# Performance work log

Hardware: AMD Instinct MI355X
Metric: run time of the kernel (lower is better)

Reference implementation:

```python
import jax, jax.numpy as jnp
import numpy as np

B, N_ATOMS, N_PROBES, N_EDGES = 4, 1250, 50000, 125000
T, D, SH_DIM, NUM_BASIS = 3, 128, 16, 10
CUTOFF = 4.0
NUM_NEIGHBORS = 20.0


def spherical_harmonics_l3(u):
    """Real spherical harmonics l=0..3, component normalization (||Y_l||^2 = 2l+1 on unit vectors). u: [E,3] unit vectors."""
    x, y, z = u[:, 0], u[:, 1], u[:, 2]
    x2, y2, z2 = x * x, y * y, z * z
    s3 = np.sqrt(3.0)
    s15 = np.sqrt(15.0)
    sh = [
        jnp.ones_like(x),                       # l=0
        s3 * x, s3 * y, s3 * z,                 # l=1
        s15 * x * y,                            # l=2
        s15 * y * z,
        (np.sqrt(5.0) / 2.0) * (3.0 * z2 - 1.0),
        s15 * x * z,
        (s15 / 2.0) * (x2 - y2),
        np.sqrt(35.0 / 8.0) * y * (3.0 * x2 - y2),   # l=3
        np.sqrt(105.0) * x * y * z,
        np.sqrt(21.0 / 8.0) * y * (5.0 * z2 - 1.0),
        (np.sqrt(7.0) / 2.0) * (5.0 * z2 * z - 3.0 * z),
        np.sqrt(21.0 / 8.0) * x * (5.0 * z2 - 1.0),
        (np.sqrt(105.0) / 2.0) * z * (x2 - y2),
        np.sqrt(35.0 / 8.0) * x * (x2 - 3.0 * y2),
    ]
    return jnp.stack(sh, axis=-1)  # [E, 16]


def radial_basis(r):
    """Normalized gaussian radial basis on [0, CUTOFF] (e3nn soft_one_hot_linspace style). r: [E]."""
    centers = jnp.linspace(0.0, CUTOFF, NUM_BASIS)
    step = CUTOFF / (NUM_BASIS - 1)
    diff = (r[:, None] - centers) / step
    return jnp.exp(-diff * diff) * 1.12  # [E, NUM_BASIS]


def setup_inputs() -> dict:
    key = jax.random.key(0)
    ks = jax.random.split(key, 10)
    atom_xyz = 6.0 * jax.random.uniform(ks[0], (B, N_ATOMS, 3), jnp.float32)
    probe_xyz = 6.0 * jax.random.uniform(ks[1], (B, N_PROBES, 3), jnp.float32)
    src = jax.random.randint(ks[2], (B, N_EDGES, 1), 0, N_ATOMS)
    dst = jax.random.randint(ks[3], (B, N_EDGES, 1), 0, N_PROBES)
    probe_edges = jnp.concatenate([src, dst], axis=-1).astype(jnp.int32)
    ped = jax.random.randint(ks[4], (B, N_EDGES, 3), -1, 2).astype(jnp.float32)
    cell = jnp.broadcast_to(6.0 * jnp.eye(3, dtype=jnp.float32), (B, 3, 3)) \
        + 0.05 * jax.random.normal(ks[5], (B, 3, 3), jnp.float32)
    atom_rep = jax.random.normal(ks[6], (T, B * N_ATOMS, D), jnp.float32)
    w1 = 0.3 * jax.random.normal(ks[7], (T, NUM_BASIS, 100), jnp.float32)
    w2 = 0.1 * jax.random.normal(ks[8], (T, 100, SH_DIM), jnp.float32)
    w_out = 0.05 * jax.random.normal(ks[9], (D, 1), jnp.float32)
    return {
        "atom_xyz": atom_xyz, "probe_xyz": probe_xyz, "probe_edges": probe_edges,
        "probe_edges_displacement": ped, "cell": cell,
        "num_nodes": jnp.full((B,), N_ATOMS, jnp.int32),
        "num_probes": jnp.full((B,), N_PROBES, jnp.int32),
        "num_probe_edges": jnp.full((B,), N_EDGES, jnp.int32),
        "atom_rep": atom_rep, "w1": w1, "w2": w2, "w_out": w_out,
    }


def reference(atom_xyz, probe_xyz, probe_edges, probe_edges_displacement, cell,
              num_nodes, num_probes, num_probe_edges, atom_rep, w1, w2, w_out):
    b, n = atom_xyz.shape[:2]
    p = probe_xyz.shape[1]
    atoms = atom_xyz.reshape(-1, 3)          # [b*n, 3]  (unpad_and_cat, equal lengths)
    probes_xyz = probe_xyz.reshape(-1, 3)    # [b*p, 3]
    zero = jnp.zeros((1,), num_nodes.dtype)
    node_off = jnp.cumsum(jnp.concatenate([zero, num_nodes[:-1]]))
    probe_off = jnp.cumsum(jnp.concatenate([zero, num_probes[:-1]]))
    off = jnp.stack([node_off, probe_off], axis=-1)[:, None, :]  # [b,1,2]
    edges = (probe_edges + off).reshape(-1, 2)                   # [E,2]
    src, dst = edges[:, 0], edges[:, 1]
    # fractional shift -> cartesian displacement via per-sample cell (repeat_interleave)
    disp = jnp.einsum('bec,bcd->bed', probe_edges_displacement, cell).reshape(-1, 3)
    vec = probes_xyz[dst] - (atoms[src] + disp)                  # [E,3]
    r = jnp.linalg.norm(vec, axis=1)
    u = vec / jnp.maximum(r, 1e-9)[:, None]
    sh = spherical_harmonics_l3(u)                               # [E,16]
    rb = radial_basis(r)                                         # [E,10]
    P = probes_xyz.shape[0]
    probes = jnp.zeros((P, atom_rep.shape[-1]), atom_xyz.dtype)
    inv_sqrt_nn = 1.0 / np.sqrt(NUM_NEIGHBORS)
    for t in range(atom_rep.shape[0]):  # small fixed number of interaction layers
        h = jax.nn.silu(rb @ w1[t]) @ w2[t]          # radial MLP -> per-edge sh weights [E,16]
        scal = jnp.sum(h * sh, axis=-1)              # contract with edge attr [E]
        msg = atom_rep[t][src] * scal[:, None]       # gather + modulate [E,D]
        probes = probes + jax.ops.segment_sum(msg, dst, num_segments=P) * inv_sqrt_nn
    out = (probes @ w_out)[:, 0].reshape(b, p)       # readout 0e scalar, pad_and_stack
    return out, probes
```

## Files before the change

kernel.cpp:

```cpp
#include <hip/hip_runtime.h>
#include <math.h>

#define B_ 4
#define NA 1250
#define NP 50000
#define NE 125000
#define T_ 3
#define D_ 128
#define SHD 16
#define NB 10
#define HID 100
#define E_TOT (B_*NE)
#define P_TOT (B_*NP)
#define A_TOT (B_*NA)
#define INV_SQRT_NN 0.22360679774997896f
#define SCAN_NBLK ((P_TOT + 1023) / 1024)

#define GRID_N 8192
#define RMAX 24.0f
#define FSTR (T_*SHD)

typedef float f32x2 __attribute__((ext_vector_type(2)));

__global__ __launch_bounds__(256) void build_table_kernel(
    const float* __restrict__ w1, const float* __restrict__ w2,
    float* __restrict__ ftab)
{
    int idx = blockIdx.x*256 + threadIdx.x;
    if (idx >= T_*GRID_N) return;
    int t = idx >> 13;
    int ri = idx & (GRID_N-1);

    float r = (float)ri * (RMAX / (float)(GRID_N-1));
    float rb[NB];
    float rs = r * (9.0f / 4.0f);
    #pragma unroll
    for (int i = 0; i < NB; ++i) {
        float dif = rs - (float)i;
        rb[i] = __expf(-dif*dif) * 1.12f;
    }

    float fk[SHD];
    #pragma unroll
    for (int k = 0; k < SHD; ++k) fk[k] = 0.0f;

    for (int j = 0; j < HID; ++j) {
        float h = 0.0f;
        #pragma unroll
        for (int i = 0; i < NB; ++i)
            h += rb[i] * w1[(size_t)(t*NB + i)*HID + j];
        float s = h / (1.0f + __expf(-h));
        #pragma unroll
        for (int k = 0; k < SHD; ++k)
            fk[k] += s * w2[(size_t)(t*HID + j)*SHD + k];
    }

    float* dstp = ftab + (size_t)ri*FSTR + t*SHD;
    #pragma unroll
    for (int k = 0; k < SHD; ++k) dstp[k] = fk[k];
}

__global__ __launch_bounds__(256) void count_kernel(const int* __restrict__ probe_edges,
                                                    int* __restrict__ counts)
{
    int e = blockIdx.x*256 + threadIdx.x;
    if (e >= E_TOT) return;
    int b = e / NE;
    int dl = probe_edges[(size_t)e*2 + 1];
    atomicAdd(&counts[dl + b*NP], 1);
}

__global__ __launch_bounds__(256) void scan1_kernel(const int* __restrict__ counts,
                                                    int* __restrict__ starts,
                                                    int* __restrict__ bsums)
{
    __shared__ int sd[256];
    int base = blockIdx.x*1024 + threadIdx.x*4;
    int v0 = (base+0 < P_TOT) ? counts[base+0] : 0;
    int v1 = (base+1 < P_TOT) ? counts[base+1] : 0;
    int v2 = (base+2 < P_TOT) ? counts[base+2] : 0;
    int v3 = (base+3 < P_TOT) ? counts[base+3] : 0;
    int s = v0+v1+v2+v3;
    sd[threadIdx.x] = s;
    __syncthreads();
    for (int off = 1; off < 256; off <<= 1) {
        int t = (threadIdx.x >= off) ? sd[threadIdx.x - off] : 0;
        __syncthreads();
        sd[threadIdx.x] += t;
        __syncthreads();
    }
    int excl = sd[threadIdx.x] - s;
    if (base+0 < P_TOT) starts[base+0] = excl;
    if (base+1 < P_TOT) starts[base+1] = excl + v0;
    if (base+2 < P_TOT) starts[base+2] = excl + v0 + v1;
    if (base+3 < P_TOT) starts[base+3] = excl + v0 + v1 + v2;
    if (threadIdx.x == 255) bsums[blockIdx.x] = sd[255];
}

__global__ __launch_bounds__(256) void scan2_kernel(int* __restrict__ bsums, int n)
{
    __shared__ int sd[256];
    int s = (threadIdx.x < n) ? bsums[threadIdx.x] : 0;
    sd[threadIdx.x] = s;
    __syncthreads();
    for (int off = 1; off < 256; off <<= 1) {
        int t = (threadIdx.x >= off) ? sd[threadIdx.x - off] : 0;
        __syncthreads();
        sd[threadIdx.x] += t;
        __syncthreads();
    }
    if (threadIdx.x < n) bsums[threadIdx.x] = sd[threadIdx.x] - s;
}

__global__ __launch_bounds__(256) void scan3_kernel(int* __restrict__ starts,
                                                    const int* __restrict__ bsums)
{
    int add = bsums[blockIdx.x];
    int base = blockIdx.x*1024 + threadIdx.x*4;
    #pragma unroll
    for (int k = 0; k < 4; ++k)
        if (base+k < P_TOT) starts[base+k] += add;
}

__global__ __launch_bounds__(256) void edge_scatter_kernel(
    const float* __restrict__ atom_xyz, const float* __restrict__ probe_xyz,
    const int* __restrict__ probe_edges, const float* __restrict__ ped,
    const float* __restrict__ cell, const float* __restrict__ ftab,
    const int* __restrict__ starts, int* __restrict__ counts2,
    float4* __restrict__ edge4)
{
    int e = blockIdx.x * 256 + threadIdx.x;
    if (e >= E_TOT) return;
    int b  = e / NE;

    int sl = probe_edges[(size_t)e*2 + 0];
    int dl = probe_edges[(size_t)e*2 + 1];
    int src = sl + b * NA;
    int dst = dl + b * NP;

    float p0 = ped[(size_t)e*3 + 0];
    float p1 = ped[(size_t)e*3 + 1];
    float p2 = ped[(size_t)e*3 + 2];
    const float* cb = cell + b*9;
    float dx = p0*cb[0] + p1*cb[3] + p2*cb[6];
    float dy = p0*cb[1] + p1*cb[4] + p2*cb[7];
    float dz = p0*cb[2] + p1*cb[5] + p2*cb[8];

    float vx = probe_xyz[(size_t)dst*3+0] - (atom_xyz[(size_t)src*3+0] + dx);
    float vy = probe_xyz[(size_t)dst*3+1] - (atom_xyz[(size_t)src*3+1] + dy);
    float vz = probe_xyz[(size_t)dst*3+2] - (atom_xyz[(size_t)src*3+2] + dz);
    float r = sqrtf(vx*vx + vy*vy + vz*vz);
    float rinv = 1.0f / fmaxf(r, 1e-9f);
    float x = vx*rinv, y = vy*rinv, z = vz*rinv;
    float x2 = x*x, y2 = y*y, z2 = z*z;

    const float S3  = 1.7320508075688772f;
    const float S15 = 3.872983346207417f;
    float sh[SHD];
    sh[0]  = 1.0f;
    sh[1]  = S3 * x;
    sh[2]  = S3 * y;
    sh[3]  = S3 * z;
    sh[4]  = S15 * x * y;
    sh[5]  = S15 * y * z;
    sh[6]  = 1.118033988749895f * (3.0f*z2 - 1.0f);
    sh[7]  = S15 * x * z;
    sh[8]  = 1.9364916731037085f * (x2 - y2);
    sh[9]  = 2.091650066335189f  * y * (3.0f*x2 - y2);
    sh[10] = 10.246950765959598f * x * y * z;
    sh[11] = 1.6201851746019651f * y * (5.0f*z2 - 1.0f);
    sh[12] = 1.3228756555322954f * (5.0f*z2*z - 3.0f*z);
    sh[13] = 1.6201851746019651f * x * (5.0f*z2 - 1.0f);
    sh[14] = 5.123475382979799f  * z * (x2 - y2);
    sh[15] = 2.091650066335189f  * x * (x2 - 3.0f*y2);

    float u = r * ((float)(GRID_N-1) / RMAX);
    int i0 = (int)u;
    i0 = (i0 > GRID_N-2) ? (GRID_N-2) : i0;
    float w = u - (float)i0;
    const float* F0 = ftab + (size_t)i0 * FSTR;
    const float* F1 = F0 + FSTR;

    float sc[T_];
    #pragma unroll
    for (int t = 0; t < T_; ++t) {
        float d0 = 0.0f, d1 = 0.0f;
        #pragma unroll
        for (int k = 0; k < SHD; ++k) {
            d0 += F0[t*SHD + k] * sh[k];
            d1 += F1[t*SHD + k] * sh[k];
        }
        sc[t] = d0 + w * (d1 - d0);
    }

    int pos = starts[dst] + atomicAdd(&counts2[dst], 1);
    edge4[pos] = make_float4(sc[0], sc[1], sc[2], __int_as_float(src));
}

__global__ __launch_bounds__(256) void gather_kernel(
    const int* __restrict__ counts, const int* __restrict__ starts,
    const float4* __restrict__ edge4, const float* __restrict__ atom_rep,
    const float* __restrict__ w_out,
    float* __restrict__ out, float* __restrict__ probes)
{
    int lane = threadIdx.x & 63;
    int wv   = threadIdx.x >> 6;
    int p = blockIdx.x*4 + wv;

    int st  = __builtin_amdgcn_readfirstlane(starts[p]);
    int cnt = __builtin_amdgcn_readfirstlane(counts[p]);

    const float2* rep2 = (const float2*)atom_rep;
    const size_t TS = (size_t)A_TOT * (D_/2);

    float ax = 0.0f, ay = 0.0f;

    for (int base = 0; base < cnt; base += 4) {
        int m = cnt - base;
        float4 e0, e1, e2, e3;
        e0 = edge4[st+base];
        if (m > 1) e1 = edge4[st+base+1];
        if (m > 2) e2 = edge4[st+base+2];
        if (m > 3) e3 = edge4[st+base+3];

        float2 a00,a01,a02, a10,a11,a12, a20,a21,a22, a30,a31,a32;
        {           size_t ro = (size_t)__float_as_int(e0.w)*(D_/2) + lane;
                    a00 = rep2[ro]; a01 = rep2[TS+ro]; a02 = rep2[2*TS+ro]; }
        if (m > 1) { size_t ro = (size_t)__float_as_int(e1.w)*(D_/2) + lane;
                    a10 = rep2[ro]; a11 = rep2[TS+ro]; a12 = rep2[2*TS+ro]; }
        if (m > 2) { size_t ro = (size_t)__float_as_int(e2.w)*(D_/2) + lane;
                    a20 = rep2[ro]; a21 = rep2[TS+ro]; a22 = rep2[2*TS+ro]; }
        if (m > 3) { size_t ro = (size_t)__float_as_int(e3.w)*(D_/2) + lane;
                    a30 = rep2[ro]; a31 = rep2[TS+ro]; a32 = rep2[2*TS+ro]; }

        ax += e0.x*a00.x + e0.y*a01.x + e0.z*a02.x;
        ay += e0.x*a00.y + e0.y*a01.y + e0.z*a02.y;
        if (m > 1) { ax += e1.x*a10.x + e1.y*a11.x + e1.z*a12.x;
                     ay += e1.x*a10.y + e1.y*a11.y + e1.z*a12.y; }
        if (m > 2) { ax += e2.x*a20.x + e2.y*a21.x + e2.z*a22.x;
                     ay += e2.x*a20.y + e2.y*a21.y + e2.z*a22.y; }
        if (m > 3) { ax += e3.x*a30.x + e3.y*a31.x + e3.z*a32.x;
                     ay += e3.x*a30.y + e3.y*a31.y + e3.z*a32.y; }
    }

    ax *= INV_SQRT_NN;
    ay *= INV_SQRT_NN;

    f32x2 v; v.x = ax; v.y = ay;
    __builtin_nontemporal_store(v, (f32x2*)(probes) + (size_t)p*(D_/2) + lane);

    float ov = ax*w_out[2*lane] + ay*w_out[2*lane+1];
    #pragma unroll
    for (int off = 32; off > 0; off >>= 1) ov += __shfl_down(ov, off);
    if (lane == 0) out[p] = ov;
}

extern "C" void kernel_launch(void* const* d_in, const int* in_sizes, int n_in,
                              void* d_out, int out_size, void* d_ws, size_t ws_size,
                              hipStream_t stream) {
    const float* atom_xyz  = (const float*)d_in[0];
    const float* probe_xyz = (const float*)d_in[1];
    const int*   probe_edges = (const int*)d_in[2];
    const float* ped       = (const float*)d_in[3];
    const float* cell      = (const float*)d_in[4];
    const float* atom_rep  = (const float*)d_in[8];
    const float* w1        = (const float*)d_in[9];
    const float* w2        = (const float*)d_in[10];
    const float* w_out     = (const float*)d_in[11];

    float* out    = (float*)d_out;
    float* probes = out + P_TOT;

    float4* edge4 = (float4*)d_ws;
    float*  ftab  = (float*)(edge4 + E_TOT);
    int* counts   = (int*)(ftab + (size_t)GRID_N*FSTR);
    int* counts2  = counts + P_TOT;
    int* starts   = counts2 + P_TOT;
    int* bsums    = starts + P_TOT;

    hipMemsetAsync(counts, 0, 2*P_TOT*sizeof(int), stream);

    build_table_kernel<<<(T_*GRID_N + 255)/256, 256, 0, stream>>>(w1, w2, ftab);

    count_kernel<<<(E_TOT + 255)/256, 256, 0, stream>>>(probe_edges, counts);

    scan1_kernel<<<SCAN_NBLK, 256, 0, stream>>>(counts, starts, bsums);
    scan2_kernel<<<1, 256, 0, stream>>>(bsums, SCAN_NBLK);
    scan3_kernel<<<SCAN_NBLK, 256, 0, stream>>>(starts, bsums);

    edge_scatter_kernel<<<(E_TOT + 255)/256, 256, 0, stream>>>(
        atom_xyz, probe_xyz, probe_edges, ped, cell, ftab,
        starts, counts2, edge4);

    gather_kernel<<<P_TOT/4, 256, 0, stream>>>(
        counts, starts, edge4, atom_rep, w_out, out, probes);
}
```

Before: 306.1 us.

## Parallelize table build per wave, reuse count ranks, half-wave gather per probe

The radial table build now assigns one wavefront per table entry, splitting the 100 hidden units across lanes and reducing with xor shuffles. Previously each thread walked all 100 hidden units serially. The count kernel records each edge's atomic rank, so the scatter kernel can use it directly. This removes the second atomic pass and its memset. The gather kernel handles two probes per wave using 32 lanes each with float4 loads, cutting lane idleness for small neighbor counts, at the cost of per-lane divergent loop trip counts.

```diff
diff --git a/kernel.cpp b/kernel.cpp
--- a/kernel.cpp
+++ b/kernel.cpp
@@ -20,16 +20,17 @@
 #define RMAX 24.0f
 #define FSTR (T_*SHD)
 
-typedef float f32x2 __attribute__((ext_vector_type(2)));
+typedef float f32x4 __attribute__((ext_vector_type(4)));
 
 __global__ __launch_bounds__(256) void build_table_kernel(
     const float* __restrict__ w1, const float* __restrict__ w2,
     float* __restrict__ ftab)
 {
-    int idx = blockIdx.x*256 + threadIdx.x;
-    if (idx >= T_*GRID_N) return;
-    int t = idx >> 13;
-    int ri = idx & (GRID_N-1);
+    int gid  = blockIdx.x*256 + threadIdx.x;
+    int w    = gid >> 6;
+    int lane = gid & 63;
+    int t  = w >> 13;
+    int ri = w & (GRID_N-1);
 
     float r = (float)ri * (RMAX / (float)(GRID_N-1));
     float rb[NB];
@@ -44,30 +45,44 @@
     #pragma unroll
     for (int k = 0; k < SHD; ++k) fk[k] = 0.0f;
 
-    for (int j = 0; j < HID; ++j) {
-        float h = 0.0f;
+    if (lane < 50) {
         #pragma unroll
-        for (int i = 0; i < NB; ++i)
-            h += rb[i] * w1[(size_t)(t*NB + i)*HID + j];
-        float s = h / (1.0f + __expf(-h));
+        for (int jj = 0; jj < 2; ++jj) {
+            int j = lane + jj*50;
+            float h = 0.0f;
+            #pragma unroll
+            for (int i = 0; i < NB; ++i)
+                h += rb[i] * w1[(size_t)(t*NB + i)*HID + j];
+            float s = h / (1.0f + __expf(-h));
+            const float* c2 = w2 + (size_t)(t*HID + j)*SHD;
+            #pragma unroll
+            for (int k = 0; k < SHD; ++k) fk[k] += s * c2[k];
+        }
+    }
+
+    #pragma unroll
+    for (int mask = 1; mask < 64; mask <<= 1) {
         #pragma unroll
-        for (int k = 0; k < SHD; ++k)
-            fk[k] += s * w2[(size_t)(t*HID + j)*SHD + k];
-    }
-
-    float* dstp = ftab + (size_t)ri*FSTR + t*SHD;
-    #pragma unroll
-    for (int k = 0; k < SHD; ++k) dstp[k] = fk[k];
+        for (int k = 0; k < SHD; ++k) fk[k] += __shfl_xor(fk[k], mask);
+    }
+
+    if (lane == 0) {
+        float* dstp = ftab + (size_t)ri*FSTR + t*SHD;
+        #pragma unroll
+        for (int k = 0; k < SHD; ++k) dstp[k] = fk[k];
+    }
 }
 
 __global__ __launch_bounds__(256) void count_kernel(const int* __restrict__ probe_edges,
-                                                    int* __restrict__ counts)
+                                                    int* __restrict__ counts,
+                                                    int* __restrict__ rank)
 {
     int e = blockIdx.x*256 + threadIdx.x;
     if (e >= E_TOT) return;
     int b = e / NE;
-    int dl = probe_edges[(size_t)e*2 + 1];
-    atomicAdd(&counts[dl + b*NP], 1);
+    int2 pe = ((const int2*)probe_edges)[e];
+    int dst = pe.y + b*NP;
+    rank[e] = atomicAdd(&counts[dst], 1);
 }
 
 __global__ __launch_bounds__(256) void scan1_kernel(const int* __restrict__ counts,
@@ -126,17 +141,16 @@
     const float* __restrict__ atom_xyz, const float* __restrict__ probe_xyz,
     const int* __restrict__ probe_edges, const float* __restrict__ ped,
     const float* __restrict__ cell, const float* __restrict__ ftab,
-    const int* __restrict__ starts, int* __restrict__ counts2,
+    const int* __restrict__ starts, const int* __restrict__ rank,
     float4* __restrict__ edge4)
 {
     int e = blockIdx.x * 256 + threadIdx.x;
     if (e >= E_TOT) return;
     int b  = e / NE;
 
-    int sl = probe_edges[(size_t)e*2 + 0];
-    int dl = probe_edges[(size_t)e*2 + 1];
-    int src = sl + b * NA;
-    int dst = dl + b * NP;
+    int2 pe = ((const int2*)probe_edges)[e];
+    int src = pe.x + b * NA;
+    int dst = pe.y + b * NP;
 
     float p0 = ped[(size_t)e*3 + 0];
     float p1 = ped[(size_t)e*3 + 1];
@@ -193,7 +207,7 @@
         sc[t] = d0 + w * (d1 - d0);
     }
 
-    int pos = starts[dst] + atomicAdd(&counts2[dst], 1);
+    int pos = starts[dst] + rank[e];
     edge4[pos] = make_float4(sc[0], sc[1], sc[2], __int_as_float(src));
 }
 
@@ -204,55 +218,53 @@
     float* __restrict__ out, float* __restrict__ probes)
 {
     int lane = threadIdx.x & 63;
+    int half = lane >> 5;
+    int l    = lane & 31;
     int wv   = threadIdx.x >> 6;
-    int p = blockIdx.x*4 + wv;
-
-    int st  = __builtin_amdgcn_readfirstlane(starts[p]);
-    int cnt = __builtin_amdgcn_readfirstlane(counts[p]);
-
-    const float2* rep2 = (const float2*)atom_rep;
-    const size_t TS = (size_t)A_TOT * (D_/2);
-
-    float ax = 0.0f, ay = 0.0f;
-
-    for (int base = 0; base < cnt; base += 4) {
+    int p = blockIdx.x*8 + wv*2 + half;
+
+    int st  = starts[p];
+    int cnt = counts[p];
+
+    const float4* rep4 = (const float4*)atom_rep;
+    const size_t TS = (size_t)A_TOT * (D_/4);
+
+    float ax = 0.0f, ay = 0.0f, az = 0.0f, aw = 0.0f;
+
+    for (int base = 0; base < cnt; base += 2) {
         int m = cnt - base;
-        float4 e0, e1, e2, e3;
+        float4 e0, e1;
         e0 = edge4[st+base];
         if (m > 1) e1 = edge4[st+base+1];
-        if (m > 2) e2 = edge4[st+base+2];
-        if (m > 3) e3 = edge4[st+base+3];
-
-        float2 a00,a01,a02, a10,a11,a12, a20,a21,a22, a30,a31,a32;
-        {           size_t ro = (size_t)__float_as_int(e0.w)*(D_/2) + lane;
-                    a00 = rep2[ro]; a01 = rep2[TS+ro]; a02 = rep2[2*TS+ro]; }
-        if (m > 1) { size_t ro = (size_t)__float_as_int(e1.w)*(D_/2) + lane;
-                    a10 = rep2[ro]; a11 = rep2[TS+ro]; a12 = rep2[2*TS+ro]; }
-        if (m > 2) { size_t ro = (size_t)__float_as_int(e2.w)*(D_/2) + lane;
-                    a20 = rep2[ro]; a21 = rep2[TS+ro]; a22 = rep2[2*TS+ro]; }
-        if (m > 3) { size_t ro = (size_t)__float_as_int(e3.w)*(D_/2) + lane;
-                    a30 = rep2[ro]; a31 = rep2[TS+ro]; a32 = rep2[2*TS+ro]; }
+
+        float4 a00,a01,a02, a10,a11,a12;
+        {           size_t ro = (size_t)__float_as_int(e0.w)*(D_/4) + l;
+                    a00 = rep4[ro]; a01 = rep4[TS+ro]; a02 = rep4[2*TS+ro]; }
+        if (m > 1) { size_t ro = (size_t)__float_as_int(e1.w)*(D_/4) + l;
+                    a10 = rep4[ro]; a11 = rep4[TS+ro]; a12 = rep4[2*TS+ro]; }
 
         ax += e0.x*a00.x + e0.y*a01.x + e0.z*a02.x;
         ay += e0.x*a00.y + e0.y*a01.y + e0.z*a02.y;
-        if (m > 1) { ax += e1.x*a10.x + e1.y*a11.x + e1.z*a12.x;
-                     ay += e1.x*a10.y + e1.y*a11.y + e1.z*a12.y; }
-        if (m > 2) { ax += e2.x*a20.x + e2.y*a21.x + e2.z*a22.x;
-                     ay += e2.x*a20.y + e2.y*a21.y + e2.z*a22.y; }
-        if (m > 3) { ax += e3.x*a30.x + e3.y*a31.x + e3.z*a32.x;
-                     ay += e3.x*a30.y + e3.y*a31.y + e3.z*a32.y; }
-    }
-
-    ax *= INV_SQRT_NN;
-    ay *= INV_SQRT_NN;
-
-    f32x2 v; v.x = ax; v.y = ay;
-    __builtin_nontemporal_store(v, (f32x2*)(probes) + (size_t)p*(D_/2) + lane);
-
-    float ov = ax*w_out[2*lane] + ay*w_out[2*lane+1];
-    #pragma unroll
-    for (int off = 32; off > 0; off >>= 1) ov += __shfl_down(ov, off);
-    if (lane == 0) out[p] = ov;
+        az += e0.x*a00.z + e0.y*a01.z + e0.z*a02.z;
+        aw += e0.x*a00.w + e0.y*a01.w + e0.z*a02.w;
+        if (m > 1) {
+            ax += e1.x*a10.x + e1.y*a11.x + e1.z*a12.x;
+            ay += e1.x*a10.y + e1.y*a11.y + e1.z*a12.y;
+            az += e1.x*a10.z + e1.y*a11.z + e1.z*a12.z;
+            aw += e1.x*a10.w + e1.y*a11.w + e1.z*a12.w;
+        }
+    }
+
+    ax *= INV_SQRT_NN; ay *= INV_SQRT_NN; az *= INV_SQRT_NN; aw *= INV_SQRT_NN;
+
+    f32x4 v; v.x = ax; v.y = ay; v.z = az; v.w = aw;
+    __builtin_nontemporal_store(v, (f32x4*)(probes) + (size_t)p*(D_/4) + l);
+
+    float4 wo = ((const float4*)w_out)[l];
+    float ov = ax*wo.x + ay*wo.y + az*wo.z + aw*wo.w;
+    #pragma unroll
+    for (int off = 16; off > 0; off >>= 1) ov += __shfl_down(ov, off, 32);
+    if (l == 0) out[p] = ov;
 }
 
 extern "C" void kernel_launch(void* const* d_in, const int* in_sizes, int n_in,
@@ -274,15 +286,15 @@
     float4* edge4 = (float4*)d_ws;
     float*  ftab  = (float*)(edge4 + E_TOT);
     int* counts   = (int*)(ftab + (size_t)GRID_N*FSTR);
-    int* counts2  = counts + P_TOT;
-    int* starts   = counts2 + P_TOT;
+    int* starts   = counts + P_TOT;
     int* bsums    = starts + P_TOT;
-
-    hipMemsetAsync(counts, 0, 2*P_TOT*sizeof(int), stream);
-
-    build_table_kernel<<<(T_*GRID_N + 255)/256, 256, 0, stream>>>(w1, w2, ftab);
-
-    count_kernel<<<(E_TOT + 255)/256, 256, 0, stream>>>(probe_edges, counts);
+    int* rank     = bsums + 256;
+
+    hipMemsetAsync(counts, 0, P_TOT*sizeof(int), stream);
+
+    build_table_kernel<<<(T_*GRID_N)/4, 256, 0, stream>>>(w1, w2, ftab);
+
+    count_kernel<<<(E_TOT + 255)/256, 256, 0, stream>>>(probe_edges, counts, rank);
 
     scan1_kernel<<<SCAN_NBLK, 256, 0, stream>>>(counts, starts, bsums);
     scan2_kernel<<<1, 256, 0, stream>>>(bsums, SCAN_NBLK);
@@ -290,8 +302,8 @@
 
     edge_scatter_kernel<<<(E_TOT + 255)/256, 256, 0, stream>>>(
         atom_xyz, probe_xyz, probe_edges, ped, cell, ftab,
-        starts, counts2, edge4);
-
-    gather_kernel<<<P_TOT/4, 256, 0, stream>>>(
+        starts, rank, edge4);
+
+    gather_kernel<<<P_TOT/8, 256, 0, stream>>>(
         counts, starts, edge4, atom_rep, w_out, out, probes);
 }
```

Result: faster. 279.6 us (-8.7%).
